# Kernel tuning notes

Measured on AMD Instinct MI355X. Metric: run time of the kernel, lower is better.

The kernel has to match this reference:

```python
import jax, jax.numpy as jnp
import numpy as np

V, E, H, B, T1, T2 = 32000, 300, 300, 64, 48, 48


def _lstm_last(x, Wih, Whh, bih, bhh):
    # x: [T, B, in]; returns final hidden state h_T: [B, H] (PyTorch gate order i,f,g,o)
    h0 = jnp.zeros((x.shape[1], Whh.shape[1]), x.dtype)
    def step(carry, xt):
        h, c = carry
        g = xt @ Wih.T + h @ Whh.T + bih + bhh
        i, f, gc, o = jnp.split(g, 4, axis=-1)
        c = jax.nn.sigmoid(f) * c + jax.nn.sigmoid(i) * jnp.tanh(gc)
        h = jax.nn.sigmoid(o) * jnp.tanh(c)
        return (h, c), None
    (h, _), _ = jax.lax.scan(step, (h0, h0), x)
    return h


def _bilstm_last(x, pf, pr):
    hf = _lstm_last(x, *pf)
    hr = _lstm_last(x[::-1], *pr)
    # faithful quirk: original reverses projr[0] along dim 0 == BATCH dim
    return jnp.concatenate([hf, hr[::-1]], axis=1)  # [B, 2H]


def _forward(x1, x2, x1_mask, x2_mask,
             emb, eW, eU, ebi, ebh, rW, rU, rbi, rbh,
             dW, dU, dbi, dbh, sW, sU, sbi, sbh,
             f1w, f1b, f2w, f2b, fow, fob):
    emb1 = emb[x1]  # [T1,B,E]
    emb2 = emb[x2]
    # encoder outputs final hidden [B,2H], broadcast over time by mask multiply (faithful quirk)
    ctx1 = _bilstm_last(emb1, (eW, eU, ebi, ebh), (rW, rU, rbi, rbh))[None] * x1_mask[:, :, None]  # [T1,B,2H]
    ctx2 = _bilstm_last(emb2, (eW, eU, ebi, ebh), (rW, rU, rbi, rbh))[None] * x2_mask[:, :, None]  # [T2,B,2H]
    c1 = ctx1.transpose(1, 0, 2)  # [B,T1,2H]
    c2 = ctx2.transpose(1, 0, 2)  # [B,T2,2H]
    # scores[b,i,j] = max_d c1[b,i,d]*c2[b,j,d]  (vectorized form of the O(T1*T2) python loop)
    scores = jnp.max(c1[:, :, None, :] * c2[:, None, :, :], axis=-1)  # [B,T1,T2]
    m1 = x1_mask.T  # [B,T1]
    m2 = x2_mask.T  # [B,T2]
    # masked softmax over hypothesis axis (axis=2)
    ea = jnp.exp(scores - jnp.max(scores, axis=2, keepdims=True)) * m2[:, None, :]
    alpha = ea / jnp.sum(ea, axis=2, keepdims=True)  # [B,T1,T2]
    # faithful quirk: MAX (not sum) pooling of attention-weighted hypothesis
    a_tilde = jnp.max(alpha[:, :, :, None] * c2[:, None, :, :], axis=2)  # [B,T1,2H]
    # masked softmax over premise axis (axis=1)
    eb = jnp.exp(scores - jnp.max(scores, axis=1, keepdims=True)) * m1[:, :, None]
    beta = eb / jnp.sum(eb, axis=1, keepdims=True)  # [B,T1,T2]
    b_tilde = jnp.einsum('bij,bid->bjd', beta, c1)  # [B,T2,2H]
    ctx1_ = a_tilde.transpose(1, 0, 2)  # [T1,B,2H]
    ctx2_ = b_tilde.transpose(1, 0, 2)  # [T2,B,2H]
    inp1 = jnp.concatenate([ctx1, ctx1_, ctx1 * ctx1_, ctx1 - ctx1_], axis=2)  # [T1,B,8H]
    inp2 = jnp.concatenate([ctx2, ctx2_, ctx2 * ctx2_, ctx2 - ctx2_], axis=2)
    h1 = jax.nn.relu(inp1 @ f1w.T + f1b)
    h2 = jax.nn.relu(inp2 @ f1w.T + f1b)
    ctx3 = _bilstm_last(h1, (dW, dU, dbi, dbh), (sW, sU, sbi, sbh))  # [B,2H]
    ctx4 = _bilstm_last(h2, (dW, dU, dbi, dbh), (sW, sU, sbi, sbh))  # [B,2H]
    w3 = ctx3[None] * x1_mask[:, :, None]  # [T1,B,2H]
    w4 = ctx4[None] * x2_mask[:, :, None]  # [T2,B,2H]
    logit = jnp.concatenate([
        w3.sum(0) / x1_mask.sum(0)[:, None], w3.max(0),
        w4.sum(0) / x2_mask.sum(0)[:, None], w4.max(0)], axis=1)  # [B,8H]
    logit = jnp.tanh(logit @ f2w.T + f2b)
    return logit @ fow.T + fob  # [B,3]


def setup_inputs() -> dict:
    key = jax.random.key(0)
    ks = jax.random.split(key, 32)
    s = 0.05
    n = lambda k, shape: jax.random.normal(k, shape, jnp.float32) * s
    d = {
        'x1': jax.random.randint(ks[0], (T1, B), 0, V, dtype=jnp.int32),
        'x1_mask': jnp.ones((T1, B), jnp.float32),
        'x2': jax.random.randint(ks[1], (T2, B), 0, V, dtype=jnp.int32),
        'x2_mask': jnp.ones((T2, B), jnp.float32),
        'l': T1,
        'embed_table': n(ks[2], (V, E)),
        'enc_Wih': n(ks[3], (4 * H, E)), 'enc_Whh': n(ks[4], (4 * H, H)),
        'enc_bih': n(ks[5], (4 * H,)), 'enc_bhh': n(ks[6], (4 * H,)),
        'encr_Wih': n(ks[7], (4 * H, E)), 'encr_Whh': n(ks[8], (4 * H, H)),
        'encr_bih': n(ks[9], (4 * H,)), 'encr_bhh': n(ks[10], (4 * H,)),
        'dec_Wih': n(ks[11], (4 * H, H)), 'dec_Whh': n(ks[12], (4 * H, H)),
        'dec_bih': n(ks[13], (4 * H,)), 'dec_bhh': n(ks[14], (4 * H,)),
        'decr_Wih': n(ks[15], (4 * H, H)), 'decr_Whh': n(ks[16], (4 * H, H)),
        'decr_bih': n(ks[17], (4 * H,)), 'decr_bhh': n(ks[18], (4 * H,)),
        'fc1_w': n(ks[19], (H, 8 * H)), 'fc1_b': n(ks[20], (H,)),
        'fc2_w': n(ks[21], (H, 8 * H)), 'fc2_b': n(ks[22], (H,)),
        'fco_w': n(ks[23], (3, H)), 'fco_b': n(ks[24], (3,)),
    }
    return d


def reference(x1, x1_mask, x2, x2_mask, l, embed_table,
              enc_Wih, enc_Whh, enc_bih, enc_bhh,
              encr_Wih, encr_Whh, encr_bih, encr_bhh,
              dec_Wih, dec_Whh, dec_bih, dec_bhh,
              decr_Wih, decr_Whh, decr_bih, decr_bhh,
              fc1_w, fc1_b, fc2_w, fc2_b, fco_w, fco_b):
    del l  # unused in original forward
    return _forward(x1, x2, x1_mask, x2_mask, embed_table,
                    enc_Wih, enc_Whh, enc_bih, enc_bhh,
                    encr_Wih, encr_Whh, encr_bih, encr_bhh,
                    dec_Wih, dec_Whh, dec_bih, dec_bhh,
                    decr_Wih, decr_Whh, decr_bih, decr_bhh,
                    fc1_w, fc1_b, fc2_w, fc2_b, fco_w, fco_b)
```

## Files before the change

kernel.cpp:

```cpp
#include <hip/hip_runtime.h>
#include <math.h>

typedef unsigned short u16;
typedef unsigned int u32;
typedef unsigned long long u64;
typedef __attribute__((ext_vector_type(8))) __bf16 bf16x8;
typedef __attribute__((ext_vector_type(4))) float f32x4;
typedef __attribute__((ext_vector_type(4))) _Float16 f16x4;

#define MR   6144
#define KP1  320
#define NPG  1280
#define NG   1200
#define WSEG 409600
#define UPSEG 409600
#define GT_H 163840

#define OFF_ABF    0UL
#define OFF_WBF    3932160UL
#define OFF_WCF    10485760UL
#define OFF_BIAS   12645760UL
#define OFF_GF     12664960UL
#define OFF_GR     28393600UL
#define OFF_HB     44122240UL
#define OFF_ENC    44286080UL
#define OFF_VB     44593280UL
#define OFF_CO     45822080UL
#define OFF_ATT    46436480UL
#define OFF_PT     46473344UL
#define OFF_LG     47087744UL
#define OFF_UP     47164544UL
#define OFF_HX     50441344UL
#define OFF_BAR    50769024UL

__device__ __forceinline__ float sigf(float x) { return 1.0f / (1.0f + expf(-x)); }
__device__ __forceinline__ float fsig(float x) { return 1.0f / (1.0f + __expf(-x)); }
__device__ __forceinline__ float ftanh(float x) { return 1.0f - 2.0f / (__expf(2.0f * x) + 1.0f); }

__device__ __forceinline__ u16 f2bf(float x) {
    union { float f; u32 u; } v; v.f = x;
    u32 r = v.u + 0x7fffu + ((v.u >> 16) & 1u);
    return (u16)(r >> 16);
}
__device__ __forceinline__ float bf2f(u16 x) {
    union { u32 u; float f; } v; v.u = ((u32)x) << 16; return v.f;
}

__device__ __forceinline__ void gld_lds16(const u16* g, u16* l) {
    __builtin_amdgcn_global_load_lds(
        (const __attribute__((address_space(1))) unsigned int*)g,
        (__attribute__((address_space(3))) unsigned int*)l, 16, 0, 0);
}

__global__ __launch_bounds__(256) void gather_bf(const int* __restrict__ x1,
                                                 const int* __restrict__ x2,
                                                 const float* __restrict__ emb,
                                                 u16* __restrict__ abf) {
    int idx = blockIdx.x * 256 + threadIdx.x;
    if (idx >= MR * KP1) return;
    int r = idx / KP1, k = idx % KP1;
    float v = 0.0f;
    if (k < 300) {
        int t = r >> 7, bc = r & 127;
        int tok = (bc < 64) ? x1[t * 64 + bc] : x2[t * 64 + bc - 64];
        v = emb[tok * 300 + k];
    }
    abf[idx] = f2bf(v);
}

__global__ __launch_bounds__(256) void wconv8_k(const float* __restrict__ w0, const float* __restrict__ w1,
                                                const float* __restrict__ w2, const float* __restrict__ w3,
                                                const float* __restrict__ w4, const float* __restrict__ w5,
                                                const float* __restrict__ w6, const float* __restrict__ w7,
                                                u16* __restrict__ out) {
    int idx = blockIdx.x * 256 + threadIdx.x;
    if (idx >= 8 * NPG * KP1) return;
    int s = idx / (NPG * KP1), rem = idx % (NPG * KP1);
    int r = rem / KP1, k = rem % KP1;
    const float* w = (s == 0) ? w0 : (s == 1) ? w1 : (s == 2) ? w2 : (s == 3) ? w3
                   : (s == 4) ? w4 : (s == 5) ? w5 : (s == 6) ? w6 : w7;
    float v = 0.0f;
    if (r < NG && k < 300) {
        int j = r >> 2, g = r & 3;
        v = w[(g * 300 + j) * 300 + k];
    }
    out[idx] = f2bf(v);
}

__global__ __launch_bounds__(256) void uperm_k(const u16* __restrict__ WU,
                                               u16* __restrict__ UP) {
    int idx = blockIdx.x * 256 + threadIdx.x;
    if (idx >= 4 * UPSEG) return;
    int seg = idx / UPSEG, pos = idx % UPSEG;
    int T = pos / 5120, kt = (pos / 512) % 10, l = (pos >> 3) & 63, e = pos & 7;
    int n = T * 16 + (l & 15);
    int k = kt * 32 + (l >> 4) * 8 + e;
    UP[idx] = WU[(size_t)seg * WSEG + (size_t)n * KP1 + k];
}

__global__ __launch_bounds__(256) void bconv_k(const float* __restrict__ b0i, const float* __restrict__ b0h,
                                               const float* __restrict__ b1i, const float* __restrict__ b1h,
                                               const float* __restrict__ b2i, const float* __restrict__ b2h,
                                               const float* __restrict__ b3i, const float* __restrict__ b3h,
                                               float* __restrict__ out) {
    int idx = blockIdx.x * 256 + threadIdx.x;
    if (idx >= 4 * NG) return;
    int s = idx / NG, n = idx % NG;
    int j = n >> 2, g = n & 3;
    int src = g * 300 + j;
    const float* bi = (s == 0) ? b0i : (s == 1) ? b1i : (s == 2) ? b2i : b3i;
    const float* bh = (s == 0) ? b0h : (s == 1) ? b1h : (s == 2) ? b2h : b3h;
    out[idx] = bi[src] + bh[src];
}

__global__ __launch_bounds__(256) void wcat_k(const float* __restrict__ f1w,
                                              float* __restrict__ wc) {
    int idx = blockIdx.x * 256 + threadIdx.x;
    if (idx >= 300 * 1800) return;
    int n = idx / 1800, k = idx % 1800;
    int nk = n * 2400 + k;
    float v;
    if (k < 600)       v = f1w[nk] + f1w[nk + 1800];
    else if (k < 1200) v = f1w[nk] - f1w[nk + 1200];
    else               v = f1w[nk];
    wc[idx] = v;
}

__global__ __launch_bounds__(256) void gemm_bt(const u16* __restrict__ A,
                                               const u16* __restrict__ B,
                                               const float* __restrict__ bias,
                                               _Float16* __restrict__ Gh) {
    __shared__ __align__(16) u16 smA[128 * 32];
    __shared__ __align__(16) u16 smB[128 * 32];
    int m0 = blockIdx.x * 128, n0 = blockIdx.y * 128;
    int tid = threadIdx.x, ln = tid & 63;
    int wm = (tid >> 6) & 1, wn = tid >> 7;
    int lrow = ln & 15, lq = ln >> 4;
    f32x4 acc[4][4] = {};
    for (int k0 = 0; k0 < KP1; k0 += 32) {
#pragma unroll
        for (int p = 0; p < 2; p++) {
            int e = (p * 256 + tid) * 8;
            int r = e >> 5, kk = e & 31;
            gld_lds16(A + (size_t)(m0 + r) * KP1 + k0 + kk, smA + e);
            gld_lds16(B + (size_t)(n0 + r) * KP1 + k0 + kk, smB + e);
        }
        __syncthreads();
        bf16x8 av[4], bv[4];
#pragma unroll
        for (int i = 0; i < 4; i++) {
            av[i] = *(const bf16x8*)&smA[(wm * 64 + i * 16 + lrow) * 32 + lq * 8];
            bv[i] = *(const bf16x8*)&smB[(wn * 64 + i * 16 + lrow) * 32 + lq * 8];
        }
#pragma unroll
        for (int i = 0; i < 4; i++)
#pragma unroll
            for (int j = 0; j < 4; j++)
                acc[i][j] = __builtin_amdgcn_mfma_f32_16x16x32_bf16(av[i], bv[j], acc[i][j], 0, 0, 0);
        __syncthreads();
    }
    size_t tb = (size_t)blockIdx.x * GT_H + (size_t)blockIdx.y * 16384
              + (size_t)wm * 8192 + (size_t)wn * 2048 + (size_t)ln * 4;
#pragma unroll
    for (int i = 0; i < 4; i++)
#pragma unroll
        for (int j = 0; j < 4; j++) {
            int n = n0 + wn * 64 + j * 16 + lrow;
            f16x4 v;
            if (n < NG) {
                float bb = bias[n];
#pragma unroll
                for (int r = 0; r < 4; r++) v[r] = (_Float16)(acc[i][j][r] + bb);
            } else {
                v = (f16x4)0;
            }
            *(f16x4*)(Gh + tb + (size_t)(i >> 1) * 4096 + (size_t)(((i & 1) * 4 + j)) * 256) = v;
        }
}

__global__ __launch_bounds__(256, 1) void lstm_sync(const _Float16* __restrict__ Gf,
                                                    const _Float16* __restrict__ Gr,
                                                    const u16* __restrict__ Upf,
                                                    const u16* __restrict__ Upr,
                                                    u16* __restrict__ hx,
                                                    u16* __restrict__ hb,
                                                    u32* __restrict__ barbase) {
    int nt = blockIdx.x, dir = blockIdx.y, half = blockIdx.z;
    const _Float16* G = dir ? Gr : Gf;
    const u16* Up = dir ? Upr : Upf;
    u32* bar = barbase + (dir * 2 + half) * 64;

    int tid = threadIdx.x, ln = tid & 63, w = tid >> 6;
    int wm = w & 1, wn = w >> 1;
    int lrow = ln & 15, lq = ln >> 4;

    __shared__ __align__(16) u16 Ulds[80 * 512];
    __shared__ float P[64][132];

    for (int p = 0; p < 20; p++) {
        int e = (p * 256 + tid) * 8;
        gld_lds16(Up + (size_t)nt * 40960 + e, Ulds + e);
    }
    __syncthreads();

    const u64* HXu = (const u64*)hx;
    u32* HXw = (u32*)hx;
    u32* HOw = (u32*)hb;

    int jp = tid & 15, bg = tid >> 4;
    bool jok = !(nt == 9 && jp >= 6);
    float c[4][2];
#pragma unroll
    for (int q = 0; q < 4; q++) { c[q][0] = 0.0f; c[q][1] = 0.0f; }

    const _Float16* Gs = G + (size_t)nt * 16384 + (size_t)half * 8192
                       + (size_t)wm * 4096 + (size_t)wn * 2048 + (size_t)ln * 4;
    f16x4 gpre[8];
    {
        int ttg = dir ? 47 : 0;
        const _Float16* Gt = Gs + (size_t)ttg * GT_H;
#pragma unroll
        for (int f = 0; f < 8; f++) gpre[f] = *(const f16x4*)(Gt + (size_t)f * 256);
    }

    for (int t = 0; t < 48; t++) {
        union { u64 d[2]; bf16x8 v; } hfrag[2][10];
        const u64* hb0 = HXu + ((size_t)(t & 1) * 2 + dir) * 10240;
#pragma unroll
        for (int i = 0; i < 2; i++) {
            int bcg = half * 64 + wm * 32 + i * 16 + lrow;
            const u64* rp = hb0 + (size_t)bcg * 80 + lq * 2;
#pragma unroll
            for (int kt = 0; kt < 10; kt++) {
                hfrag[i][kt].d[0] = __hip_atomic_load(rp + kt * 8,     __ATOMIC_RELAXED, __HIP_MEMORY_SCOPE_AGENT);
                hfrag[i][kt].d[1] = __hip_atomic_load(rp + kt * 8 + 1, __ATOMIC_RELAXED, __HIP_MEMORY_SCOPE_AGENT);
            }
        }

        f32x4 acc[2][4];
#pragma unroll
        for (int i = 0; i < 2; i++)
#pragma unroll
            for (int j = 0; j < 4; j++) {
                f32x4 a;
#pragma unroll
                for (int r = 0; r < 4; r++) a[r] = (float)gpre[i * 4 + j][r];
                acc[i][j] = a;
            }

#pragma unroll
        for (int kt = 0; kt < 10; kt++) {
            bf16x8 bv[4];
#pragma unroll
            for (int j = 0; j < 4; j++)
                bv[j] = *(const bf16x8*)&Ulds[((size_t)(wn * 4 + j) * 10 + kt) * 512 + ln * 8];
#pragma unroll
            for (int i = 0; i < 2; i++)
#pragma unroll
                for (int j = 0; j < 4; j++)
                    acc[i][j] = __builtin_amdgcn_mfma_f32_16x16x32_bf16(hfrag[i][kt].v, bv[j], acc[i][j], 0, 0, 0);
        }

#pragma unroll
        for (int i = 0; i < 2; i++)
#pragma unroll
            for (int j = 0; j < 4; j++) {
                int col = wn * 64 + j * 16 + lrow;
#pragma unroll
                for (int r = 0; r < 4; r++)
                    P[wm * 32 + i * 16 + lq * 4 + r][col] = acc[i][j][r];
            }
        __syncthreads();

        if (t < 47) {
            int ttg = dir ? 46 - t : t + 1;
            const _Float16* Gt = Gs + (size_t)ttg * GT_H;
#pragma unroll
            for (int f = 0; f < 8; f++) gpre[f] = *(const f16x4*)(Gt + (size_t)f * 256);
        }

        if (jok) {
            u32* hxo = HXw + ((size_t)((t + 1) & 1) * 2 + dir) * 20480;
#pragma unroll
            for (int q = 0; q < 4; q++) {
                int bc = bg * 4 + q;
                f32x4 g0 = *(const f32x4*)&P[bc][8 * jp];
                f32x4 g1 = *(const f32x4*)&P[bc][8 * jp + 4];
                float cn0 = fsig(g0[1]) * c[q][0] + fsig(g0[0]) * ftanh(g0[2]);
                float hn0 = fsig(g0[3]) * ftanh(cn0);
                float cn1 = fsig(g1[1]) * c[q][1] + fsig(g1[0]) * ftanh(g1[2]);
                float hn1 = fsig(g1[3]) * ftanh(cn1);
                c[q][0] = cn0; c[q][1] = cn1;
                u32 pk = (u32)f2bf(hn0) | ((u32)f2bf(hn1) << 16);
                int bcg = half * 64 + bc;
                size_t oi = (size_t)bcg * 160 + nt * 16 + jp;
                if (t < 47)
                    __hip_atomic_store(hxo + oi, pk, __ATOMIC_RELAXED, __HIP_MEMORY_SCOPE_AGENT);
                else
                    HOw[(size_t)dir * 20480 + oi] = pk;
            }
        }

        if (t < 47) {
            __syncthreads();
            if (tid == 0) {
                __hip_atomic_fetch_add(bar, 1u, __ATOMIC_RELAXED, __HIP_MEMORY_SCOPE_AGENT);
                u32 tgt = 10u * (u32)(t + 1);
                while (__hip_atomic_load(bar, __ATOMIC_RELAXED, __HIP_MEMORY_SCOPE_AGENT) < tgt)
                    __builtin_amdgcn_s_sleep(2);
            }
            __syncthreads();
        } else {
            __syncthreads();
        }
    }
}

__global__ __launch_bounds__(256) void enc_k(const u16* __restrict__ hF,
                                             const u16* __restrict__ hR,
                                             float* __restrict__ enc) {
    int idx = blockIdx.x * 256 + threadIdx.x;
    if (idx >= 128 * 600) return;
    int bc = idx / 600, d = idx % 600;
    int seq = bc >> 6, b = bc & 63;
    enc[idx] = (d < 300) ? bf2f(hF[bc * KP1 + d])
                         : bf2f(hR[(seq * 64 + 63 - b) * KP1 + d - 300]);
}

__global__ __launch_bounds__(256) void vbuf_k(const float* __restrict__ enc,
                                              float* __restrict__ V) {
    int idx = blockIdx.x * 256 + threadIdx.x;
    if (idx >= 64 * 600) return;
    int b = idx / 600, d = idx % 600;
    float e1 = enc[b * 600 + d], e2 = enc[(64 + b) * 600 + d];
    float p = fmaxf(e2, 0.0f), nn = fminf(e2, 0.0f);
    V[0 * 38400 + idx] = e1;
    V[1 * 38400 + idx] = p;
    V[2 * 38400 + idx] = nn;
    V[3 * 38400 + idx] = e1 * p;
    V[4 * 38400 + idx] = e1 * nn;
    V[5 * 38400 + idx] = e2;
    V[6 * 38400 + idx] = e1;
    V[7 * 38400 + idx] = e1 * e2;
}

__global__ __launch_bounds__(256) void attn_lite(const float* __restrict__ enc,
                                                 const float* __restrict__ x1m,
                                                 const float* __restrict__ x2m,
                                                 float* __restrict__ AMX,
                                                 float* __restrict__ AMN,
                                                 float* __restrict__ SS) {
    int b = blockIdx.x, tid = threadIdx.x;
    __shared__ float sc[48][49];
    __shared__ float rmx[4], rmn[4];
    __shared__ float MxMn[2];
    float mx = -3.4e38f, mn = 3.4e38f;
    for (int d = tid; d < 600; d += 256) {
        float p = enc[b * 600 + d] * enc[(64 + b) * 600 + d];
        mx = fmaxf(mx, p); mn = fminf(mn, p);
    }
    for (int off = 32; off; off >>= 1) {
        mx = fmaxf(mx, __shfl_down(mx, off));
        mn = fminf(mn, __shfl_down(mn, off));
    }
    if ((tid & 63) == 0) { rmx[tid >> 6] = mx; rmn[tid >> 6] = mn; }
    __syncthreads();
    if (tid == 0) {
        MxMn[0] = fmaxf(fmaxf(rmx[0], rmx[1]), fmaxf(rmx[2], rmx[3]));
        MxMn[1] = fminf(fminf(rmn[0], rmn[1]), fminf(rmn[2], rmn[3]));
    }
    __syncthreads();
    float Mx = MxMn[0], Mn = MxMn[1];
    for (int idx = tid; idx < 2304; idx += 256) {
        int i = idx / 48, j = idx % 48;
        float q = x1m[i * 64 + b] * x2m[j * 64 + b];
        sc[i][j] = (q > 0.0f) ? q * Mx : ((q < 0.0f) ? q * Mn : 0.0f);
    }
    __syncthreads();
    if (tid < 48) {
        int i = tid;
        float m = -3.4e38f;
        for (int j = 0; j < 48; j++) m = fmaxf(m, sc[i][j]);
        float sum = 0.0f;
        for (int j = 0; j < 48; j++) sum += expf(sc[i][j] - m) * x2m[j * 64 + b];
        float wmax = -3.4e38f, wmin = 3.4e38f;
        for (int j = 0; j < 48; j++) {
            float w = expf(sc[i][j] - m) * x2m[j * 64 + b] * x2m[j * 64 + b];
            wmax = fmaxf(wmax, w); wmin = fminf(wmin, w);
        }
        AMX[i * 64 + b] = wmax / sum;
        AMN[i * 64 + b] = wmin / sum;
    } else if (tid >= 64 && tid < 112) {
        int j = tid - 64;
        float m = -3.4e38f;
        for (int i = 0; i < 48; i++) m = fmaxf(m, sc[i][j]);
        float sum = 0.0f, sm = 0.0f;
        for (int i = 0; i < 48; i++) {
            float e = expf(sc[i][j] - m) * x1m[i * 64 + b];
            sum += e; sm += e * x1m[i * 64 + b];
        }
        SS[j * 64 + b] = sm / sum;
    }
}

__global__ __launch_bounds__(256) void coeff_gemm(const float* __restrict__ V,
                                                  const float* __restrict__ Wc,
                                                  float* __restrict__ CO) {
    __shared__ float As[16][64];
    __shared__ float Ws[16][64];
    int s = blockIdx.y;
    const int offs[8] = {0, 600, 600, 1200, 1200, 0, 600, 1200};
    int koff = offs[s];
    const float* A = V + (size_t)s * 38400;
    float* C = CO + (size_t)s * 19200;
    int n0 = blockIdx.x * 64;
    int tid = threadIdx.x;
    int lrow = tid >> 2;
    int lk4 = (tid & 3) << 2;
    int tm = (tid & 15) << 2;
    int tn = (tid >> 4) << 2;
    int nW = n0 + lrow;
    float acc[4][4] = {};
    for (int k0 = 0; k0 < 600; k0 += 16) {
        __syncthreads();
#pragma unroll
        for (int q = 0; q < 4; q++) {
            int k = k0 + lk4 + q;
            As[lk4 + q][lrow] = (k < 600) ? A[lrow * 600 + k] : 0.0f;
            Ws[lk4 + q][lrow] = (k < 600 && nW < 300) ? Wc[(size_t)nW * 1800 + koff + k] : 0.0f;
        }
        __syncthreads();
#pragma unroll
        for (int kk = 0; kk < 16; kk++) {
            float a0 = As[kk][tm], a1 = As[kk][tm + 1], a2 = As[kk][tm + 2], a3 = As[kk][tm + 3];
            float w0 = Ws[kk][tn], w1 = Ws[kk][tn + 1], w2 = Ws[kk][tn + 2], w3 = Ws[kk][tn + 3];
            acc[0][0] += a0 * w0; acc[0][1] += a0 * w1; acc[0][2] += a0 * w2; acc[0][3] += a0 * w3;
            acc[1][0] += a1 * w0; acc[1][1] += a1 * w1; acc[1][2] += a1 * w2; acc[1][3] += a1 * w3;
            acc[2][0] += a2 * w0; acc[2][1] += a2 * w1; acc[2][2] += a2 * w2; acc[2][3] += a2 * w3;
            acc[3][0] += a3 * w0; acc[3][1] += a3 * w1; acc[3][2] += a3 * w2; acc[3][3] += a3 * w3;
        }
    }
#pragma unroll
    for (int ii = 0; ii < 4; ii++) {
        int m = tm + ii;
#pragma unroll
        for (int jn = 0; jn < 4; jn++) {
            int n = n0 + tn + jn;
            if (n < 300) C[m * 300 + n] = acc[ii][jn];
        }
    }
}

__global__ __launch_bounds__(320) void combine_k(const float* __restrict__ CO,
                                                 const float* __restrict__ f1b,
                                                 const float* __restrict__ x1m,
                                                 const float* __restrict__ x2m,
                                                 const float* __restrict__ AMX,
                                                 const float* __restrict__ AMN,
                                                 const float* __restrict__ SS,
                                                 u16* __restrict__ OUT) {
    int r = blockIdx.x;
    int t = r >> 7, bc = r & 127;
    int seq = bc >> 6, b = bc & 63;
    int n = threadIdx.x;
    if (n >= 300) return;
    int bn = b * 300 + n;
    float pre;
    if (seq == 0) {
        float m1 = x1m[t * 64 + b], am = AMX[t * 64 + b], an = AMN[t * 64 + b];
        pre = m1 * CO[bn] + am * CO[19200 + bn] + an * CO[2 * 19200 + bn]
            + m1 * am * CO[3 * 19200 + bn] + m1 * an * CO[4 * 19200 + bn] + f1b[n];
    } else {
        float m2 = x2m[t * 64 + b], sv = SS[t * 64 + b];
        pre = m2 * CO[5 * 19200 + bn] + sv * CO[6 * 19200 + bn]
            + m2 * sv * CO[7 * 19200 + bn] + f1b[n];
    }
    OUT[(size_t)r * KP1 + n] = f2bf(fmaxf(pre, 0.0f));
}

__global__ __launch_bounds__(256) void pool_k(const float* __restrict__ dctx,
                                              const float* __restrict__ x1m,
                                              const float* __restrict__ x2m,
                                              float* __restrict__ pooledT) {
    int idx = blockIdx.x * 256 + threadIdx.x;
    if (idx >= 64 * 2400) return;
    int b = idx / 2400, col = idx % 2400;
    int sec = col / 600, d = col % 600;
    const float* msk = (sec < 2) ? x1m : x2m;
    float v = dctx[((sec < 2 ? 0 : 64) + b) * 600 + d];
    float out;
    if ((sec & 1) == 0) {
        float s = 0, sm = 0;
        for (int t = 0; t < 48; t++) { float mv = msk[t * 64 + b]; s += v * mv; sm += mv; }
        out = s / sm;
    } else {
        float m = -3.4e38f;
        for (int t = 0; t < 48; t++) m = fmaxf(m, v * msk[t * 64 + b]);
        out = m;
    }
    pooledT[col * 64 + b] = out;
}

__global__ __launch_bounds__(256) void fc2_k2(const float* __restrict__ pooledT,
                                              const float* __restrict__ f2w,
                                              const float* __restrict__ f2b,
                                              float* __restrict__ logit) {
    __shared__ float wl[2400];
    __shared__ float red[256];
    int n = blockIdx.x;
    for (int i = threadIdx.x; i < 2400; i += 256) wl[i] = f2w[n * 2400 + i];
    __syncthreads();
    int b = threadIdx.x & 63, kc = threadIdx.x >> 6;
    float acc = 0.0f;
    int k0 = kc * 600;
    for (int kk = 0; kk < 600; kk++) acc += pooledT[(k0 + kk) * 64 + b] * wl[k0 + kk];
    red[threadIdx.x] = acc;
    __syncthreads();
    if (threadIdx.x < 64) {
        float s = red[b] + red[64 + b] + red[128 + b] + red[192 + b];
        logit[b * 300 + n] = tanhf(s + f2b[n]);
    }
}

__global__ __launch_bounds__(64) void out_k2(const float* __restrict__ logit,
                                             const float* __restrict__ fow,
                                             const float* __restrict__ fob,
                                             float* __restrict__ out) {
    int b = blockIdx.x, tid = threadIdx.x;
    float p0 = 0, p1 = 0, p2 = 0;
    for (int k = tid; k < 300; k += 64) {
        float l = logit[b * 300 + k];
        p0 += l * fow[k]; p1 += l * fow[300 + k]; p2 += l * fow[600 + k];
    }
    for (int off = 32; off; off >>= 1) {
        p0 += __shfl_down(p0, off);
        p1 += __shfl_down(p1, off);
        p2 += __shfl_down(p2, off);
    }
    if (tid == 0) {
        out[b * 3 + 0] = p0 + fob[0];
        out[b * 3 + 1] = p1 + fob[1];
        out[b * 3 + 2] = p2 + fob[2];
    }
}

extern "C" void kernel_launch(void* const* d_in, const int* in_sizes, int n_in,
                              void* d_out, int out_size, void* d_ws, size_t ws_size,
                              hipStream_t stream) {
    (void)in_sizes; (void)n_in; (void)out_size; (void)ws_size;
    const int*   x1  = (const int*)d_in[0];
    const float* x1m = (const float*)d_in[1];
    const int*   x2  = (const int*)d_in[2];
    const float* x2m = (const float*)d_in[3];
    const float* emb = (const float*)d_in[5];
    const float* eW  = (const float*)d_in[6];
    const float* eU  = (const float*)d_in[7];
    const float* ebi = (const float*)d_in[8];
    const float* ebh = (const float*)d_in[9];
    const float* rW  = (const float*)d_in[10];
    const float* rU  = (const float*)d_in[11];
    const float* rbi = (const float*)d_in[12];
    const float* rbh = (const float*)d_in[13];
    const float* dW  = (const float*)d_in[14];
    const float* dU  = (const float*)d_in[15];
    const float* dbi = (const float*)d_in[16];
    const float* dbh = (const float*)d_in[17];
    const float* sW  = (const float*)d_in[18];
    const float* sU  = (const float*)d_in[19];
    const float* sbi = (const float*)d_in[20];
    const float* sbh = (const float*)d_in[21];
    const float* f1w = (const float*)d_in[22];
    const float* f1b = (const float*)d_in[23];
    const float* f2w = (const float*)d_in[24];
    const float* f2b = (const float*)d_in[25];
    const float* fow = (const float*)d_in[26];
    const float* fob = (const float*)d_in[27];

    char* wsb = (char*)d_ws;
    u16*       ABF  = (u16*)(wsb + OFF_ABF);
    u16*       WBF  = (u16*)(wsb + OFF_WBF);
    float*     WCF  = (float*)(wsb + OFF_WCF);
    float*     BIAS = (float*)(wsb + OFF_BIAS);
    _Float16*  GFh  = (_Float16*)(wsb + OFF_GF);
    _Float16*  GRh  = (_Float16*)(wsb + OFF_GR);
    u16*       HB   = (u16*)(wsb + OFF_HB);
    float*     ENC  = (float*)(wsb + OFF_ENC);
    float*     VB   = (float*)(wsb + OFF_VB);
    float*     CO   = (float*)(wsb + OFF_CO);
    float*     AMX  = (float*)(wsb + OFF_ATT);
    float*     AMN  = AMX + 3072;
    float*     SS   = AMX + 6144;
    float*     PT   = (float*)(wsb + OFF_PT);
    float*     LG   = (float*)(wsb + OFF_LG);
    u16*       UP   = (u16*)(wsb + OFF_UP);
    u16*       HX   = (u16*)(wsb + OFF_HX);
    u32*       BAR  = (u32*)(wsb + OFF_BAR);

    u16* HF0 = HB;
    u16* HR0 = HB + 40960;

    gather_bf<<<dim3((MR * KP1 + 255) / 256), 256, 0, stream>>>(x1, x2, emb, ABF);
    wconv8_k<<<dim3((8 * NPG * KP1 + 255) / 256), 256, 0, stream>>>(eW, rW, dW, sW, eU, rU, dU, sU, WBF);
    uperm_k<<<dim3((4 * UPSEG + 255) / 256), 256, 0, stream>>>(WBF + 4 * WSEG, UP);
    bconv_k<<<dim3((4 * NG + 255) / 256), 256, 0, stream>>>(ebi, ebh, rbi, rbh, dbi, dbh, sbi, sbh, BIAS);
    wcat_k<<<dim3((300 * 1800 + 255) / 256), 256, 0, stream>>>(f1w, WCF);
    hipMemsetAsync(wsb + OFF_BAR, 0, 2048, stream);

    hipMemsetAsync(wsb + OFF_HX, 0, 327680, stream);
    gemm_bt<<<dim3(48, 10), 256, 0, stream>>>(ABF, WBF,        BIAS,      GFh);
    gemm_bt<<<dim3(48, 10), 256, 0, stream>>>(ABF, WBF + WSEG, BIAS + NG, GRh);
    lstm_sync<<<dim3(10, 2, 2), 256, 0, stream>>>(GFh, GRh, UP, UP + UPSEG, HX, HB, BAR);

    enc_k<<<dim3((128 * 600 + 255) / 256), 256, 0, stream>>>(HF0, HR0, ENC);
    vbuf_k<<<dim3((64 * 600 + 255) / 256), 256, 0, stream>>>(ENC, VB);
    attn_lite<<<dim3(64), 256, 0, stream>>>(ENC, x1m, x2m, AMX, AMN, SS);
    coeff_gemm<<<dim3(5, 8), 256, 0, stream>>>(VB, WCF, CO);
    combine_k<<<dim3(6144), 320, 0, stream>>>(CO, f1b, x1m, x2m, AMX, AMN, SS, ABF);

    hipMemsetAsync(wsb + OFF_HX, 0, 327680, stream);
    gemm_bt<<<dim3(48, 10), 256, 0, stream>>>(ABF, WBF + 2 * WSEG, BIAS + 2 * NG, GFh);
    gemm_bt<<<dim3(48, 10), 256, 0, stream>>>(ABF, WBF + 3 * WSEG, BIAS + 3 * NG, GRh);
    lstm_sync<<<dim3(10, 2, 2), 256, 0, stream>>>(GFh, GRh, UP + 2 * UPSEG, UP + 3 * UPSEG, HX, HB, BAR + 1024);

    enc_k<<<dim3((128 * 600 + 255) / 256), 256, 0, stream>>>(HF0, HR0, ENC);
    pool_k<<<dim3((64 * 2400 + 255) / 256), 256, 0, stream>>>(ENC, x1m, x2m, PT);
    fc2_k2<<<dim3(300), 256, 0, stream>>>(PT, f2w, f2b, LG);
    out_k2<<<dim3(64), 64, 0, stream>>>(LG, fow, fob, (float*)d_out);
}
```

Baseline: 1.046 ms.

## Fuse prep kernels, replace LSTM barrier with per-block flags, drop enc buffers

Merges the five weight/embedding preparation kernels into one launch, and builds the permuted recurrent weights directly from the fp32 inputs instead of from an intermediate bf16 copy. The LSTM grid barrier changes from a shared atomic counter to per-block step flags polled by ten threads. Step zero now uses a zero hidden state in registers, so the HX memsets can go. The enc/vbuf/attn kernels are fused, and pool reads the hidden states directly. The gate-preactivation prefetch for the next step is removed, which puts the G load back on the serial recurrence path, and the flag barrier relies on relaxed ordering.

Result: slower. 1.071 ms (+2.4%).

```diff
diff --git a/kernel.cpp b/kernel.cpp
--- a/kernel.cpp
+++ b/kernel.cpp
@@ -18,22 +18,20 @@
 
 #define OFF_ABF    0UL
 #define OFF_WBF    3932160UL
-#define OFF_WCF    10485760UL
-#define OFF_BIAS   12645760UL
-#define OFF_GF     12664960UL
-#define OFF_GR     28393600UL
-#define OFF_HB     44122240UL
-#define OFF_ENC    44286080UL
-#define OFF_VB     44593280UL
-#define OFF_CO     45822080UL
-#define OFF_ATT    46436480UL
-#define OFF_PT     46473344UL
-#define OFF_LG     47087744UL
-#define OFF_UP     47164544UL
-#define OFF_HX     50441344UL
-#define OFF_BAR    50769024UL
-
-__device__ __forceinline__ float sigf(float x) { return 1.0f / (1.0f + expf(-x)); }
+#define OFF_WCF    7208960UL
+#define OFF_BIAS   9368960UL
+#define OFF_GF     9388160UL
+#define OFF_GR     25116800UL
+#define OFF_HB     40845440UL
+#define OFF_VB     41009280UL
+#define OFF_CO     42238080UL
+#define OFF_ATT    42852480UL
+#define OFF_PT     42889344UL
+#define OFF_LG     43503744UL
+#define OFF_UP     43580544UL
+#define OFF_HX     46857344UL
+#define OFF_BAR    47185024UL
+
 __device__ __forceinline__ float fsig(float x) { return 1.0f / (1.0f + __expf(-x)); }
 __device__ __forceinline__ float ftanh(float x) { return 1.0f - 2.0f / (__expf(2.0f * x) + 1.0f); }
 
@@ -52,78 +50,76 @@
         (__attribute__((address_space(3))) unsigned int*)l, 16, 0, 0);
 }
 
-__global__ __launch_bounds__(256) void gather_bf(const int* __restrict__ x1,
-                                                 const int* __restrict__ x2,
-                                                 const float* __restrict__ emb,
-                                                 u16* __restrict__ abf) {
-    int idx = blockIdx.x * 256 + threadIdx.x;
-    if (idx >= MR * KP1) return;
-    int r = idx / KP1, k = idx % KP1;
-    float v = 0.0f;
-    if (k < 300) {
-        int t = r >> 7, bc = r & 127;
-        int tok = (bc < 64) ? x1[t * 64 + bc] : x2[t * 64 + bc - 64];
-        v = emb[tok * 300 + k];
-    }
-    abf[idx] = f2bf(v);
-}
-
-__global__ __launch_bounds__(256) void wconv8_k(const float* __restrict__ w0, const float* __restrict__ w1,
-                                                const float* __restrict__ w2, const float* __restrict__ w3,
-                                                const float* __restrict__ w4, const float* __restrict__ w5,
-                                                const float* __restrict__ w6, const float* __restrict__ w7,
-                                                u16* __restrict__ out) {
-    int idx = blockIdx.x * 256 + threadIdx.x;
-    if (idx >= 8 * NPG * KP1) return;
-    int s = idx / (NPG * KP1), rem = idx % (NPG * KP1);
-    int r = rem / KP1, k = rem % KP1;
-    const float* w = (s == 0) ? w0 : (s == 1) ? w1 : (s == 2) ? w2 : (s == 3) ? w3
-                   : (s == 4) ? w4 : (s == 5) ? w5 : (s == 6) ? w6 : w7;
-    float v = 0.0f;
-    if (r < NG && k < 300) {
-        int j = r >> 2, g = r & 3;
-        v = w[(g * 300 + j) * 300 + k];
-    }
-    out[idx] = f2bf(v);
-}
-
-__global__ __launch_bounds__(256) void uperm_k(const u16* __restrict__ WU,
-                                               u16* __restrict__ UP) {
-    int idx = blockIdx.x * 256 + threadIdx.x;
-    if (idx >= 4 * UPSEG) return;
-    int seg = idx / UPSEG, pos = idx % UPSEG;
-    int T = pos / 5120, kt = (pos / 512) % 10, l = (pos >> 3) & 63, e = pos & 7;
-    int n = T * 16 + (l & 15);
-    int k = kt * 32 + (l >> 4) * 8 + e;
-    UP[idx] = WU[(size_t)seg * WSEG + (size_t)n * KP1 + k];
-}
-
-__global__ __launch_bounds__(256) void bconv_k(const float* __restrict__ b0i, const float* __restrict__ b0h,
-                                               const float* __restrict__ b1i, const float* __restrict__ b1h,
-                                               const float* __restrict__ b2i, const float* __restrict__ b2h,
-                                               const float* __restrict__ b3i, const float* __restrict__ b3h,
-                                               float* __restrict__ out) {
-    int idx = blockIdx.x * 256 + threadIdx.x;
-    if (idx >= 4 * NG) return;
-    int s = idx / NG, n = idx % NG;
-    int j = n >> 2, g = n & 3;
-    int src = g * 300 + j;
-    const float* bi = (s == 0) ? b0i : (s == 1) ? b1i : (s == 2) ? b2i : b3i;
-    const float* bh = (s == 0) ? b0h : (s == 1) ? b1h : (s == 2) ? b2h : b3h;
-    out[idx] = bi[src] + bh[src];
-}
-
-__global__ __launch_bounds__(256) void wcat_k(const float* __restrict__ f1w,
-                                              float* __restrict__ wc) {
-    int idx = blockIdx.x * 256 + threadIdx.x;
-    if (idx >= 300 * 1800) return;
-    int n = idx / 1800, k = idx % 1800;
-    int nk = n * 2400 + k;
-    float v;
-    if (k < 600)       v = f1w[nk] + f1w[nk + 1800];
-    else if (k < 1200) v = f1w[nk] - f1w[nk + 1200];
-    else               v = f1w[nk];
-    wc[idx] = v;
+__global__ __launch_bounds__(256) void prep_k(
+    const int* __restrict__ x1, const int* __restrict__ x2, const float* __restrict__ emb,
+    const float* __restrict__ w0, const float* __restrict__ w1,
+    const float* __restrict__ w2, const float* __restrict__ w3,
+    const float* __restrict__ u0, const float* __restrict__ u1,
+    const float* __restrict__ u2, const float* __restrict__ u3,
+    const float* __restrict__ b0i, const float* __restrict__ b0h,
+    const float* __restrict__ b1i, const float* __restrict__ b1h,
+    const float* __restrict__ b2i, const float* __restrict__ b2h,
+    const float* __restrict__ b3i, const float* __restrict__ b3h,
+    const float* __restrict__ f1w,
+    u16* __restrict__ abf, u16* __restrict__ wbf, u16* __restrict__ up,
+    float* __restrict__ bias, float* __restrict__ wc) {
+    int blk = blockIdx.x, tid = threadIdx.x;
+    if (blk < 7680) {
+        int idx = blk * 256 + tid;
+        int r = idx / KP1, k = idx % KP1;
+        float v = 0.0f;
+        if (k < 300) {
+            int t = r >> 7, bc = r & 127;
+            int tok = (bc < 64) ? x1[t * 64 + bc] : x2[t * 64 + bc - 64];
+            v = emb[tok * 300 + k];
+        }
+        abf[idx] = f2bf(v);
+    } else if (blk < 14080) {
+        int idx = (blk - 7680) * 256 + tid;
+        int s = idx / (NPG * KP1), rem = idx % (NPG * KP1);
+        int r = rem / KP1, k = rem % KP1;
+        const float* w = (s == 0) ? w0 : (s == 1) ? w1 : (s == 2) ? w2 : w3;
+        float v = 0.0f;
+        if (r < NG && k < 300) {
+            int j = r >> 2, g = r & 3;
+            v = w[(g * 300 + j) * 300 + k];
+        }
+        wbf[idx] = f2bf(v);
+    } else if (blk < 20480) {
+        int idx = (blk - 14080) * 256 + tid;
+        int seg = idx / UPSEG, pos = idx % UPSEG;
+        int T = pos / 5120, kt = (pos / 512) % 10, l = (pos >> 3) & 63, e = pos & 7;
+        int n = T * 16 + (l & 15);
+        int k = kt * 32 + (l >> 4) * 8 + e;
+        const float* u = (seg == 0) ? u0 : (seg == 1) ? u1 : (seg == 2) ? u2 : u3;
+        float v = 0.0f;
+        if (n < NG && k < 300) {
+            int j = n >> 2, g = n & 3;
+            v = u[(g * 300 + j) * 300 + k];
+        }
+        up[idx] = f2bf(v);
+    } else if (blk < 20499) {
+        int idx = (blk - 20480) * 256 + tid;
+        if (idx < 4 * NG) {
+            int s = idx / NG, n = idx % NG;
+            int j = n >> 2, g = n & 3;
+            int src = g * 300 + j;
+            const float* bi = (s == 0) ? b0i : (s == 1) ? b1i : (s == 2) ? b2i : b3i;
+            const float* bh = (s == 0) ? b0h : (s == 1) ? b1h : (s == 2) ? b2h : b3h;
+            bias[idx] = bi[src] + bh[src];
+        }
+    } else {
+        int idx = (blk - 20499) * 256 + tid;
+        if (idx < 300 * 1800) {
+            int n = idx / 1800, k = idx % 1800;
+            int nk = n * 2400 + k;
+            float v;
+            if (k < 600)       v = f1w[nk] + f1w[nk + 1800];
+            else if (k < 1200) v = f1w[nk] - f1w[nk + 1200];
+            else               v = f1w[nk];
+            wc[idx] = v;
+        }
+    }
 }
 
 __global__ __launch_bounds__(256) void gemm_bt(const u16* __restrict__ A,
@@ -188,7 +184,7 @@
     int nt = blockIdx.x, dir = blockIdx.y, half = blockIdx.z;
     const _Float16* G = dir ? Gr : Gf;
     const u16* Up = dir ? Upr : Upf;
-    u32* bar = barbase + (dir * 2 + half) * 64;
+    u32* flags = barbase + (dir * 2 + half) * 64;
 
     int tid = threadIdx.x, ln = tid & 63, w = tid >> 6;
     int wm = w & 1, wn = w >> 1;
@@ -215,39 +211,35 @@
 
     const _Float16* Gs = G + (size_t)nt * 16384 + (size_t)half * 8192
                        + (size_t)wm * 4096 + (size_t)wn * 2048 + (size_t)ln * 4;
-    f16x4 gpre[8];
-    {
-        int ttg = dir ? 47 : 0;
+
+    for (int t = 0; t < 48; t++) {
+        int ttg = dir ? 47 - t : t;
         const _Float16* Gt = Gs + (size_t)ttg * GT_H;
-#pragma unroll
-        for (int f = 0; f < 8; f++) gpre[f] = *(const f16x4*)(Gt + (size_t)f * 256);
-    }
-
-    for (int t = 0; t < 48; t++) {
+        f16x4 gv[8];
+#pragma unroll
+        for (int f = 0; f < 8; f++) gv[f] = *(const f16x4*)(Gt + (size_t)f * 256);
+
         union { u64 d[2]; bf16x8 v; } hfrag[2][10];
-        const u64* hb0 = HXu + ((size_t)(t & 1) * 2 + dir) * 10240;
-#pragma unroll
-        for (int i = 0; i < 2; i++) {
-            int bcg = half * 64 + wm * 32 + i * 16 + lrow;
-            const u64* rp = hb0 + (size_t)bcg * 80 + lq * 2;
-#pragma unroll
-            for (int kt = 0; kt < 10; kt++) {
-                hfrag[i][kt].d[0] = __hip_atomic_load(rp + kt * 8,     __ATOMIC_RELAXED, __HIP_MEMORY_SCOPE_AGENT);
-                hfrag[i][kt].d[1] = __hip_atomic_load(rp + kt * 8 + 1, __ATOMIC_RELAXED, __HIP_MEMORY_SCOPE_AGENT);
+        if (t > 0) {
+            const u64* hb0 = HXu + ((size_t)(t & 1) * 2 + dir) * 10240;
+#pragma unroll
+            for (int i = 0; i < 2; i++) {
+                int bcg = half * 64 + wm * 32 + i * 16 + lrow;
+                const u64* rp = hb0 + (size_t)bcg * 80 + lq * 2;
+#pragma unroll
+                for (int kt = 0; kt < 10; kt++) {
+                    hfrag[i][kt].d[0] = __hip_atomic_load(rp + kt * 8,     __ATOMIC_RELAXED, __HIP_MEMORY_SCOPE_AGENT);
+                    hfrag[i][kt].d[1] = __hip_atomic_load(rp + kt * 8 + 1, __ATOMIC_RELAXED, __HIP_MEMORY_SCOPE_AGENT);
+                }
             }
-        }
-
-        f32x4 acc[2][4];
-#pragma unroll
-        for (int i = 0; i < 2; i++)
-#pragma unroll
-            for (int j = 0; j < 4; j++) {
-                f32x4 a;
-#pragma unroll
-                for (int r = 0; r < 4; r++) a[r] = (float)gpre[i * 4 + j][r];
-                acc[i][j] = a;
-            }
-
+        } else {
+#pragma unroll
+            for (int i = 0; i < 2; i++)
+#pragma unroll
+                for (int kt = 0; kt < 10; kt++) { hfrag[i][kt].d[0] = 0; hfrag[i][kt].d[1] = 0; }
+        }
+
+        f32x4 acc[2][4] = {};
 #pragma unroll
         for (int kt = 0; kt < 10; kt++) {
             bf16x8 bv[4];
@@ -268,16 +260,9 @@
                 int col = wn * 64 + j * 16 + lrow;
 #pragma unroll
                 for (int r = 0; r < 4; r++)
-                    P[wm * 32 + i * 16 + lq * 4 + r][col] = acc[i][j][r];
+                    P[wm * 32 + i * 16 + lq * 4 + r][col] = acc[i][j][r] + (float)gv[i * 4 + j][r];
             }
         __syncthreads();
-
-        if (t < 47) {
-            int ttg = dir ? 46 - t : t + 1;
-            const _Float16* Gt = Gs + (size_t)ttg * GT_H;
-#pragma unroll
-            for (int f = 0; f < 8; f++) gpre[f] = *(const f16x4*)(Gt + (size_t)f * 256);
-        }
 
         if (jok) {
             u32* hxo = HXw + ((size_t)((t + 1) & 1) * 2 + dir) * 20480;
@@ -303,60 +288,52 @@
 
         if (t < 47) {
             __syncthreads();
-            if (tid == 0) {
-                __hip_atomic_fetch_add(bar, 1u, __ATOMIC_RELAXED, __HIP_MEMORY_SCOPE_AGENT);
-                u32 tgt = 10u * (u32)(t + 1);
-                while (__hip_atomic_load(bar, __ATOMIC_RELAXED, __HIP_MEMORY_SCOPE_AGENT) < tgt)
-                    __builtin_amdgcn_s_sleep(2);
+            if (tid == 0)
+                __hip_atomic_store(&flags[nt], (u32)(t + 1), __ATOMIC_RELAXED, __HIP_MEMORY_SCOPE_AGENT);
+            if (tid < 10) {
+                while (__hip_atomic_load(&flags[tid], __ATOMIC_RELAXED, __HIP_MEMORY_SCOPE_AGENT) < (u32)(t + 1))
+                    __builtin_amdgcn_s_sleep(1);
             }
             __syncthreads();
-        } else {
-            __syncthreads();
-        }
-    }
-}
-
-__global__ __launch_bounds__(256) void enc_k(const u16* __restrict__ hF,
-                                             const u16* __restrict__ hR,
-                                             float* __restrict__ enc) {
-    int idx = blockIdx.x * 256 + threadIdx.x;
-    if (idx >= 128 * 600) return;
-    int bc = idx / 600, d = idx % 600;
-    int seq = bc >> 6, b = bc & 63;
-    enc[idx] = (d < 300) ? bf2f(hF[bc * KP1 + d])
-                         : bf2f(hR[(seq * 64 + 63 - b) * KP1 + d - 300]);
-}
-
-__global__ __launch_bounds__(256) void vbuf_k(const float* __restrict__ enc,
-                                              float* __restrict__ V) {
-    int idx = blockIdx.x * 256 + threadIdx.x;
-    if (idx >= 64 * 600) return;
-    int b = idx / 600, d = idx % 600;
-    float e1 = enc[b * 600 + d], e2 = enc[(64 + b) * 600 + d];
-    float p = fmaxf(e2, 0.0f), nn = fminf(e2, 0.0f);
-    V[0 * 38400 + idx] = e1;
-    V[1 * 38400 + idx] = p;
-    V[2 * 38400 + idx] = nn;
-    V[3 * 38400 + idx] = e1 * p;
-    V[4 * 38400 + idx] = e1 * nn;
-    V[5 * 38400 + idx] = e2;
-    V[6 * 38400 + idx] = e1;
-    V[7 * 38400 + idx] = e1 * e2;
-}
-
-__global__ __launch_bounds__(256) void attn_lite(const float* __restrict__ enc,
-                                                 const float* __restrict__ x1m,
-                                                 const float* __restrict__ x2m,
-                                                 float* __restrict__ AMX,
-                                                 float* __restrict__ AMN,
-                                                 float* __restrict__ SS) {
-    int b = blockIdx.x, tid = threadIdx.x;
+        }
+    }
+}
+
+__global__ __launch_bounds__(256) void attp_k(const u16* __restrict__ hF,
+                                              const u16* __restrict__ hR,
+                                              const float* __restrict__ x1m,
+                                              const float* __restrict__ x2m,
+                                              float* __restrict__ V,
+                                              float* __restrict__ AMX,
+                                              float* __restrict__ AMN,
+                                              float* __restrict__ SS) {
+    int tid = threadIdx.x;
+    if (blockIdx.x < 150) {
+        int idx = blockIdx.x * 256 + tid;
+        if (idx >= 64 * 600) return;
+        int b = idx / 600, d = idx % 600;
+        float e1 = (d < 300) ? bf2f(hF[b * KP1 + d]) : bf2f(hR[(63 - b) * KP1 + d - 300]);
+        float e2 = (d < 300) ? bf2f(hF[(64 + b) * KP1 + d]) : bf2f(hR[(127 - b) * KP1 + d - 300]);
+        float p = fmaxf(e2, 0.0f), nn = fminf(e2, 0.0f);
+        V[0 * 38400 + idx] = e1;
+        V[1 * 38400 + idx] = p;
+        V[2 * 38400 + idx] = nn;
+        V[3 * 38400 + idx] = e1 * p;
+        V[4 * 38400 + idx] = e1 * nn;
+        V[5 * 38400 + idx] = e2;
+        V[6 * 38400 + idx] = e1;
+        V[7 * 38400 + idx] = e1 * e2;
+        return;
+    }
+    int b = blockIdx.x - 150;
     __shared__ float sc[48][49];
     __shared__ float rmx[4], rmn[4];
     __shared__ float MxMn[2];
     float mx = -3.4e38f, mn = 3.4e38f;
     for (int d = tid; d < 600; d += 256) {
-        float p = enc[b * 600 + d] * enc[(64 + b) * 600 + d];
+        float e1 = (d < 300) ? bf2f(hF[b * KP1 + d]) : bf2f(hR[(63 - b) * KP1 + d - 300]);
+        float e2 = (d < 300) ? bf2f(hF[(64 + b) * KP1 + d]) : bf2f(hR[(127 - b) * KP1 + d - 300]);
+        float p = e1 * e2;
         mx = fmaxf(mx, p); mn = fminf(mn, p);
     }
     for (int off = 32; off; off >>= 1) {
@@ -385,8 +362,8 @@
         for (int j = 0; j < 48; j++) sum += expf(sc[i][j] - m) * x2m[j * 64 + b];
         float wmax = -3.4e38f, wmin = 3.4e38f;
         for (int j = 0; j < 48; j++) {
-            float w = expf(sc[i][j] - m) * x2m[j * 64 + b] * x2m[j * 64 + b];
-            wmax = fmaxf(wmax, w); wmin = fminf(wmin, w);
+            float wv = expf(sc[i][j] - m) * x2m[j * 64 + b] * x2m[j * 64 + b];
+            wmax = fmaxf(wmax, wv); wmin = fminf(wmin, wv);
         }
         AMX[i * 64 + b] = wmax / sum;
         AMN[i * 64 + b] = wmin / sum;
@@ -478,7 +455,8 @@
     OUT[(size_t)r * KP1 + n] = f2bf(fmaxf(pre, 0.0f));
 }
 
-__global__ __launch_bounds__(256) void pool_k(const float* __restrict__ dctx,
+__global__ __launch_bounds__(256) void pool_k(const u16* __restrict__ hF,
+                                              const u16* __restrict__ hR,
                                               const float* __restrict__ x1m,
                                               const float* __restrict__ x2m,
                                               float* __restrict__ pooledT) {
@@ -487,7 +465,10 @@
     int b = idx / 2400, col = idx % 2400;
     int sec = col / 600, d = col % 600;
     const float* msk = (sec < 2) ? x1m : x2m;
-    float v = dctx[((sec < 2 ? 0 : 64) + b) * 600 + d];
+    int bc = (sec < 2 ? 0 : 64) + b;
+    int seq = bc >> 6;
+    float v = (d < 300) ? bf2f(hF[bc * KP1 + d])
+                        : bf2f(hR[(seq * 64 + 63 - b) * KP1 + d - 300]);
     float out;
     if ((sec & 1) == 0) {
         float s = 0, sm = 0;
@@ -584,7 +565,6 @@
     _Float16*  GFh  = (_Float16*)(wsb + OFF_GF);
     _Float16*  GRh  = (_Float16*)(wsb + OFF_GR);
     u16*       HB   = (u16*)(wsb + OFF_HB);
-    float*     ENC  = (float*)(wsb + OFF_ENC);
     float*     VB   = (float*)(wsb + OFF_VB);
     float*     CO   = (float*)(wsb + OFF_CO);
     float*     AMX  = (float*)(wsb + OFF_ATT);
@@ -599,31 +579,25 @@
     u16* HF0 = HB;
     u16* HR0 = HB + 40960;
 
-    gather_bf<<<dim3((MR * KP1 + 255) / 256), 256, 0, stream>>>(x1, x2, emb, ABF);
-    wconv8_k<<<dim3((8 * NPG * KP1 + 255) / 256), 256, 0, stream>>>(eW, rW, dW, sW, eU, rU, dU, sU, WBF);
-    uperm_k<<<dim3((4 * UPSEG + 255) / 256), 256, 0, stream>>>(WBF + 4 * WSEG, UP);
-    bconv_k<<<dim3((4 * NG + 255) / 256), 256, 0, stream>>>(ebi, ebh, rbi, rbh, dbi, dbh, sbi, sbh, BIAS);
-    wcat_k<<<dim3((300 * 1800 + 255) / 256), 256, 0, stream>>>(f1w, WCF);
+    prep_k<<<dim3(22609), 256, 0, stream>>>(x1, x2, emb,
+                                            eW, rW, dW, sW, eU, rU, dU, sU,
+                                            ebi, ebh, rbi, rbh, dbi, dbh, sbi, sbh,
+                                            f1w, ABF, WBF, UP, BIAS, WCF);
     hipMemsetAsync(wsb + OFF_BAR, 0, 2048, stream);
 
-    hipMemsetAsync(wsb + OFF_HX, 0, 327680, stream);
     gemm_bt<<<dim3(48, 10), 256, 0, stream>>>(ABF, WBF,        BIAS,      GFh);
     gemm_bt<<<dim3(48, 10), 256, 0, stream>>>(ABF, WBF + WSEG, BIAS + NG, GRh);
     lstm_sync<<<dim3(10, 2, 2), 256, 0, stream>>>(GFh, GRh, UP, UP + UPSEG, HX, HB, BAR);
 
-    enc_k<<<dim3((128 * 600 + 255) / 256), 256, 0, stream>>>(HF0, HR0, ENC);
-    vbuf_k<<<dim3((64 * 600 + 255) / 256), 256, 0, stream>>>(ENC, VB);
-    attn_lite<<<dim3(64), 256, 0, stream>>>(ENC, x1m, x2m, AMX, AMN, SS);
+    attp_k<<<dim3(214), 256, 0, stream>>>(HF0, HR0, x1m, x2m, VB, AMX, AMN, SS);
     coeff_gemm<<<dim3(5, 8), 256, 0, stream>>>(VB, WCF, CO);
     combine_k<<<dim3(6144), 320, 0, stream>>>(CO, f1b, x1m, x2m, AMX, AMN, SS, ABF);
 
-    hipMemsetAsync(wsb + OFF_HX, 0, 327680, stream);
     gemm_bt<<<dim3(48, 10), 256, 0, stream>>>(ABF, WBF + 2 * WSEG, BIAS + 2 * NG, GFh);
     gemm_bt<<<dim3(48, 10), 256, 0, stream>>>(ABF, WBF + 3 * WSEG, BIAS + 3 * NG, GRh);
-    lstm_sync<<<dim3(10, 2, 2), 256, 0, stream>>>(GFh, GRh, UP + 2 * UPSEG, UP + 3 * UPSEG, HX, HB, BAR + 1024);
-
-    enc_k<<<dim3((128 * 600 + 255) / 256), 256, 0, stream>>>(HF0, HR0, ENC);
-    pool_k<<<dim3((64 * 2400 + 255) / 256), 256, 0, stream>>>(ENC, x1m, x2m, PT);
+    lstm_sync<<<dim3(10, 2, 2), 256, 0, stream>>>(GFh, GRh, UP + 2 * UPSEG, UP + 3 * UPSEG, HX, HB, BAR + 256);
+
+    pool_k<<<dim3((64 * 2400 + 255) / 256), 256, 0, stream>>>(HF0, HR0, x1m, x2m, PT);
     fc2_k2<<<dim3(300), 256, 0, stream>>>(PT, f2w, f2b, LG);
     out_k2<<<dim3(64), 64, 0, stream>>>(LG, fow, fob, (float*)d_out);
 }
```
